# Kernel optimization log

Measured on AMD Instinct MI355X. Metric: run time of the kernel, lower is better.

Reference implementation:

```python
import jax, jax.numpy as jnp
import numpy as np

N, E, H, L, R, NG = 8192, 131072, 256, 3, 128, 64
NUM_ELEMENTS = 80
CUTOFF = 12.0
INV_SQRT_2 = 1.0 / np.sqrt(2.0)
INV_SQRT_3 = 1.0 / np.sqrt(3.0)
INV_SQRT_H = 1.0 / np.sqrt(H)


def _glorot(key, shape):
    fan_in, fan_out = shape[-2], shape[-1]
    return jax.random.normal(key, shape, jnp.float32) * np.sqrt(2.0 / (fan_in + fan_out))


def setup_inputs():
    key = jax.random.key(0)
    ks = jax.random.split(key, 24)
    pos = jax.random.normal(ks[0], (N, 3), jnp.float32) * 5.0
    z = jax.random.randint(ks[1], (N,), 0, NUM_ELEMENTS)
    src = jax.random.randint(ks[2], (E,), 0, N)
    off = jax.random.randint(ks[3], (E,), 1, N)
    dst = (src + off) % N  # guarantee no self-loops (dist > 0)
    edge_index = jnp.stack([src, dst])
    batch = jnp.sort(jax.random.randint(ks[4], (N,), 0, NG))
    return {
        "pos": pos,
        "atom_emb": jax.random.normal(ks[5], (NUM_ELEMENTS, H), jnp.float32),
        "ln_w": jnp.ones((L, H), jnp.float32),
        "ln_b": jnp.zeros((L, H), jnp.float32),
        "xp_w1": _glorot(ks[6], (L, H, H)),
        "xp_b1": jnp.zeros((L, H), jnp.float32),
        "xp_w2": _glorot(ks[7], (L, H, 3 * H)),
        "xp_b2": jnp.zeros((L, 3 * H), jnp.float32),
        "rbf_w": _glorot(ks[8], (L, R, 3 * H)),
        "rbf_b": jnp.zeros((L, 3 * H), jnp.float32),
        "vec_w": _glorot(ks[9], (L, H, 2 * H)),
        "xv_w1": _glorot(ks[10], (L, 2 * H, H)),
        "xv_b1": jnp.zeros((L, H), jnp.float32),
        "xv_w2": _glorot(ks[11], (L, H, 3 * H)),
        "xv_b2": jnp.zeros((L, 3 * H), jnp.float32),
        "oe_w1": _glorot(ks[12], (H, H // 2)),
        "oe_b1": jnp.zeros((H // 2,), jnp.float32),
        "oe_w2": _glorot(ks[13], (H // 2, 1)),
        "oe_b2": jnp.zeros((1,), jnp.float32),
        "z": z,
        "edge_index": edge_index,
        "batch": batch,
    }


def _gaussian_rbf(dist):
    offset = jnp.linspace(0.0, CUTOFF, R)
    coeff = -0.5 / (offset[1] - offset[0]) ** 2
    return jnp.exp(coeff * (dist[:, None] - offset[None, :]) ** 2)  # [E, R]


def _layernorm(x, w, b):
    mu = x.mean(-1, keepdims=True)
    var = x.var(-1, keepdims=True)
    return (x - mu) / jnp.sqrt(var + 1e-5) * w + b


def reference(pos, atom_emb, ln_w, ln_b, xp_w1, xp_b1, xp_w2, xp_b2,
              rbf_w, rbf_b, vec_w, xv_w1, xv_b1, xv_w2, xv_b2,
              oe_w1, oe_b1, oe_w2, oe_b2, z, edge_index, batch):
    src, dst = edge_index[0], edge_index[1]
    rel = pos[src] - pos[dst]                       # [E, 3]
    dist = jnp.sqrt((rel ** 2).sum(-1))             # [E]
    edge_rbf = _gaussian_rbf(dist)                  # [E, R]
    edge_vector = rel / dist[:, None]               # [E, 3] unit vectors

    x = atom_emb[z]                                 # [N, H]
    vec = jnp.zeros((N, 3, H), x.dtype)

    for l in range(L):
        # ---- PaiNNMessage ----
        xh = _layernorm(x, ln_w[l], ln_b[l])
        xh = jax.nn.silu(xh @ xp_w1[l] + xp_b1[l]) @ xp_w2[l] + xp_b2[l]  # [N, 3H]
        rbfh = edge_rbf @ rbf_w[l] + rbf_b[l]                             # [E, 3H]
        m = xh[src] * rbfh
        mx, xh2, xh3 = jnp.split(m, 3, axis=-1)
        xh2 = xh2 * INV_SQRT_3
        mvec = (vec[src] * xh2[:, None, :] + xh3[:, None, :] * edge_vector[:, :, None]) * INV_SQRT_H
        dx = jax.ops.segment_sum(mx, dst, num_segments=N)
        dvec = jax.ops.segment_sum(mvec, dst, num_segments=N)
        x = (x + dx) * INV_SQRT_2
        vec = vec + dvec

        # ---- PaiNNUpdate ----
        vp = vec @ vec_w[l]                          # [N, 3, 2H]
        vec1, vec2 = jnp.split(vp, 2, axis=-1)
        vec_dot = (vec1 * vec2).sum(axis=1) * INV_SQRT_H           # [N, H]
        vnorm = jnp.sqrt((vec2 ** 2).sum(axis=1) + 1e-8)           # [N, H]
        h = jnp.concatenate([x, vnorm], axis=-1)
        h = jax.nn.silu(h @ xv_w1[l] + xv_b1[l]) @ xv_w2[l] + xv_b2[l]
        xv1, xv2, xv3 = jnp.split(h, 3, axis=-1)
        dx = (xv1 + xv2 * vec_dot) * INV_SQRT_2
        dvec = xv3[:, None, :] * vec1
        x = (x + dx) * INV_SQRT_2
        vec = vec + dvec

    # ---- energy head: per-atom MLP then per-molecule sum ----
    per_atom = jax.nn.silu(x @ oe_w1 + oe_b1) @ oe_w2 + oe_b2      # [N, 1]
    energy = jax.ops.segment_sum(per_atom, batch, num_segments=NG)  # [NG, 1]
    return energy
```

## Files before the change

### kernel.cpp

```cpp
#include <hip/hip_runtime.h>
#include <hip/hip_bf16.h>
#include <math.h>

#define NN 8192
#define EE 131072
#define HH 256
#define LL 3
#define RR 128
#define NGG 64
#define MSG_WAVES 16

typedef __attribute__((ext_vector_type(8))) short bf16x8;
typedef __attribute__((ext_vector_type(4))) float f32x4;
typedef unsigned short u16;

union U4 { ushort4 v; unsigned short a[4]; };
union U8 { uint4 v; unsigned short a[8]; };

__device__ __forceinline__ float silu(float v) { return v / (1.0f + expf(-v)); }
__device__ __forceinline__ float b2f(unsigned short u) { return __uint_as_float(((unsigned)u) << 16); }
__device__ __forceinline__ unsigned short f2b(float f) {
    unsigned u = __float_as_uint(f);
    u += 0x7fff + ((u >> 16) & 1);
    return (unsigned short)(u >> 16);
}

constexpr float kInvSqrt2 = 0.70710678118654752440f;
constexpr float kInvSqrt3 = 0.57735026918962576451f;
constexpr float kInvSqrtH = 0.0625f;

__global__ void k_zero(float* __restrict__ p, int n4) {
    int i = blockIdx.x * 256 + threadIdx.x;
    if (i < n4) ((float4*)p)[i] = make_float4(0.f, 0.f, 0.f, 0.f);
}

__global__ __launch_bounds__(256) void k_wt_all(
    const float* __restrict__ xp_w1, const float* __restrict__ xp_w2,
    const float* __restrict__ rbf_w, const float* __restrict__ vec_w,
    const float* __restrict__ xv_w1, const float* __restrict__ xv_w2,
    const float* __restrict__ oe_w1,
    u16* __restrict__ xp_w1T, u16* __restrict__ xp_w2T, u16* __restrict__ rbf_wKb,
    u16* __restrict__ vec_wT, u16* __restrict__ xv_w1T, u16* __restrict__ xv_w2T,
    u16* __restrict__ oe_w1T) {
    int bid = blockIdx.x;
    const float* src; u16* dst; int K, N, t, cast = 0;
    if (bid < 2400) {
        int l = bid / 800, r = bid % 800;
        if (r < 64)       { src = xp_w1 + (size_t)l * 65536;  dst = xp_w1T + (size_t)l * 65536;  K = 256; N = 256; t = r; }
        else if (r < 256) { src = xp_w2 + (size_t)l * 196608; dst = xp_w2T + (size_t)l * 196608; K = 256; N = 768; t = r - 64; }
        else if (r < 352) { src = rbf_w + (size_t)l * 98304;  dst = rbf_wKb + (size_t)l * 98304; K = 128; N = 768; t = r - 256; cast = 1; }
        else if (r < 480) { src = vec_w + (size_t)l * 131072; dst = vec_wT + (size_t)l * 131072; K = 256; N = 512; t = r - 352; }
        else if (r < 608) { src = xv_w1 + (size_t)l * 131072; dst = xv_w1T + (size_t)l * 131072; K = 512; N = 256; t = r - 480; }
        else              { src = xv_w2 + (size_t)l * 196608; dst = xv_w2T + (size_t)l * 196608; K = 256; N = 768; t = r - 608; }
    } else {
        src = oe_w1; dst = oe_w1T; K = 256; N = 128; t = bid - 2400;
    }
    int nx = N >> 5;
    int bn = (t % nx) * 32, bk = (t / nx) * 32;
    int tx = threadIdx.x & 31, ty = threadIdx.x >> 5;
    if (cast) {
#pragma unroll
        for (int i = 0; i < 32; i += 8)
            dst[(size_t)(bk + ty + i) * N + bn + tx] = f2b(src[(size_t)(bk + ty + i) * N + bn + tx]);
        return;
    }
    __shared__ float tile[32][33];
#pragma unroll
    for (int i = 0; i < 32; i += 8)
        tile[ty + i][tx] = src[(size_t)(bk + ty + i) * N + bn + tx];
    __syncthreads();
#pragma unroll
    for (int i = 0; i < 32; i += 8)
        dst[(size_t)(bn + ty + i) * K + bk + tx] = f2b(tile[tx][ty + i]);
}

__global__ void k_init_ln(const float* __restrict__ emb, const int* __restrict__ z,
                          const float* __restrict__ w, const float* __restrict__ b,
                          float* __restrict__ x, u16* __restrict__ xlnb) {
    int n = blockIdx.x, t = threadIdx.x;
    float v = emb[z[n] * HH + t];
    x[(size_t)n * HH + t] = v;
    float s = v, q = v * v;
#pragma unroll
    for (int m = 32; m >= 1; m >>= 1) {
        s += __shfl_xor(s, m, 64);
        q += __shfl_xor(q, m, 64);
    }
    __shared__ float s_sum[4], s_sq[4];
    int wid = t >> 6;
    if ((t & 63) == 0) { s_sum[wid] = s; s_sq[wid] = q; }
    __syncthreads();
    float S = s_sum[0] + s_sum[1] + s_sum[2] + s_sum[3];
    float Q = s_sq[0] + s_sq[1] + s_sq[2] + s_sq[3];
    float mu = S * (1.0f / HH);
    float var = Q * (1.0f / HH) - mu * mu;
    float rs = rsqrtf(var + 1e-5f);
    xlnb[(size_t)n * HH + t] = f2b((v - mu) * rs * w[t] + b[t]);
}

__global__ void k_edge_geom(const float* __restrict__ pos, const int* __restrict__ ei,
                            float* __restrict__ ev ) {
    int e = blockIdx.x * 256 + threadIdx.x;
    if (e >= EE) return;
    int s = ei[e], d = ei[EE + e];
    float rx = pos[s * 3 + 0] - pos[d * 3 + 0];
    float ry = pos[s * 3 + 1] - pos[d * 3 + 1];
    float rz = pos[s * 3 + 2] - pos[d * 3 + 2];
    float dist = sqrtf(rx * rx + ry * ry + rz * rz);
    float inv = 1.0f / dist;
    ((float4*)ev)[e] = make_float4(rx * inv, ry * inv, rz * inv, dist);
}

__global__ void k_hist(const int* __restrict__ ei, int* __restrict__ deg) {
    int e = blockIdx.x * 256 + threadIdx.x;
    if (e < EE) atomicAdd(&deg[ei[EE + e]], 1);
}
__global__ void k_scan(const int* __restrict__ deg, int* __restrict__ row_ptr,
                       int* __restrict__ fill) {
    __shared__ int buf[256];
    __shared__ int carry_s;
    int t = threadIdx.x;
    if (t == 0) carry_s = 0;
    __syncthreads();
    for (int r = 0; r < NN; r += 256) {
        int v = deg[r + t];
        buf[t] = v;
        __syncthreads();
        for (int ofs = 1; ofs < 256; ofs <<= 1) {
            int add = (t >= ofs) ? buf[t - ofs] : 0;
            __syncthreads();
            buf[t] += add;
            __syncthreads();
        }
        int excl = buf[t] - v;
        int carry = carry_s;
        row_ptr[r + t] = carry + excl;
        fill[r + t] = carry + excl;
        __syncthreads();
        if (t == 255) carry_s = carry + buf[t];
        __syncthreads();
    }
    if (t == 0) row_ptr[NN] = carry_s;
}
__global__ void k_sort(const int* __restrict__ deg, int* __restrict__ dorder) {
    __shared__ int bins[256];
    __shared__ int base[256];
    int t = threadIdx.x;
    bins[t] = 0;
    __syncthreads();
    for (int d = t; d < NN; d += 256) {
        int b = deg[d]; b = b > 255 ? 255 : b;
        atomicAdd(&bins[b], 1);
    }
    __syncthreads();
    if (t == 0) {
        int acc = 0;
        for (int k = 255; k >= 0; --k) { base[k] = acc; acc += bins[k]; }
    }
    __syncthreads();
    bins[t] = 0;
    __syncthreads();
    for (int d = t; d < NN; d += 256) {
        int b = deg[d]; b = b > 255 ? 255 : b;
        int p = atomicAdd(&bins[b], 1);
        dorder[base[b] + p] = d;
    }
}
__global__ void k_scatter(const int* __restrict__ ei, const float* __restrict__ ev,
                          int* __restrict__ fill, int* __restrict__ srcp,
                          float4* __restrict__ evp, int* __restrict__ k0tab,
                          float* __restrict__ gtab) {
    int e = blockIdx.x * 256 + threadIdx.x;
    if (e >= EE) return;
    int d = ei[EE + e];
    int pos = atomicAdd(&fill[d], 1);
    float4 e4 = ((const float4*)ev)[e];
    srcp[pos] = ei[e];
    evp[pos] = e4;
    const float step = 12.0f / 127.0f;
    const float coeff = -0.5f / (step * step);
    float dist = e4.w;
    int k0 = (int)floorf(dist / step) - 3;
    k0 = k0 < 0 ? 0 : (k0 > 120 ? 120 : k0);
    float g[8];
#pragma unroll
    for (int k = 0; k < 8; ++k) {
        float t = dist - (k0 + k) * step;
        g[k] = expf(coeff * t * t);
    }
    k0tab[pos] = k0;
    ((float4*)gtab)[pos * 2 + 0] = make_float4(g[0], g[1], g[2], g[3]);
    ((float4*)gtab)[pos * 2 + 1] = make_float4(g[4], g[5], g[6], g[7]);
}

template <int AF32, int OUT_BF16, int ACT>
__global__ __launch_bounds__(256) void k_gemm(
    const void* __restrict__ Av, const u16* __restrict__ BT,
    const float* __restrict__ bias, void* __restrict__ C, int M, int K, int N) {
    __shared__ uint4 As4[512];
    __shared__ uint4 Bs4[512];
    u16* As = (u16*)As4;
    u16* Bs = (u16*)Bs4;
    int tid = threadIdx.x;
    int wave = tid >> 6, lane = tid & 63;
    int bm = blockIdx.y * 128, bn = blockIdx.x * 128;
    int wm = (wave >> 1) * 64, wn = (wave & 1) * 64;
    int lm = lane & 15;
    int kg = lane >> 4;
    f32x4 acc[4][4] = {};

    for (int k0 = 0; k0 < K; k0 += 32) {
#pragma unroll
        for (int it = 0; it < 2; ++it) {
            int idx = it * 256 + tid;
            int r = idx >> 2, seg = idx & 3;
            if (AF32) {
                const float* Af = (const float*)Av;
                float4 fa = *(const float4*)&Af[(size_t)(bm + r) * K + k0 + seg * 8];
                float4 fb = *(const float4*)&Af[(size_t)(bm + r) * K + k0 + seg * 8 + 4];
                U8 u;
                u.a[0] = f2b(fa.x); u.a[1] = f2b(fa.y); u.a[2] = f2b(fa.z); u.a[3] = f2b(fa.w);
                u.a[4] = f2b(fb.x); u.a[5] = f2b(fb.y); u.a[6] = f2b(fb.z); u.a[7] = f2b(fb.w);
                As4[idx] = u.v;
            } else {
                const u16* A = (const u16*)Av;
                As4[idx] = *(const uint4*)&A[(size_t)(bm + r) * K + k0 + seg * 8];
            }
            Bs4[idx] = *(const uint4*)&BT[(size_t)(bn + r) * K + k0 + seg * 8];
        }
        __syncthreads();
        bf16x8 af[4], bfr[4];
#pragma unroll
        for (int i = 0; i < 4; ++i)
            af[i] = *(const bf16x8*)&As[(wm + i * 16 + lm) * 32 + kg * 8];
#pragma unroll
        for (int j = 0; j < 4; ++j)
            bfr[j] = *(const bf16x8*)&Bs[(wn + j * 16 + lm) * 32 + kg * 8];
#pragma unroll
        for (int i = 0; i < 4; ++i)
#pragma unroll
            for (int j = 0; j < 4; ++j)
                acc[i][j] = __builtin_amdgcn_mfma_f32_16x16x32_bf16(af[i], bfr[j], acc[i][j], 0, 0, 0);
        __syncthreads();
    }

#pragma unroll
    for (int j = 0; j < 4; ++j) {
        int col = bn + wn + j * 16 + lm;
        float bv = bias ? bias[col] : 0.f;
#pragma unroll
        for (int i = 0; i < 4; ++i) {
            int row0 = bm + wm + i * 16 + kg * 4;
#pragma unroll
            for (int r = 0; r < 4; ++r) {
                float v = acc[i][j][r] + bv;
                if (ACT) v = silu(v);
                if (OUT_BF16)
                    ((u16*)C)[(size_t)(row0 + r) * N + col] = f2b(v);
                else
                    ((float*)C)[(size_t)(row0 + r) * N + col] = v;
            }
        }
    }
}

__global__ __launch_bounds__(1024) void k_msg(
    const u16* __restrict__ xhb, const u16* __restrict__ vinb,
    const int* __restrict__ srcp, const float4* __restrict__ evp,
    const int* __restrict__ row_ptr, const int* __restrict__ k0tab,
    const float* __restrict__ gtab, const u16* __restrict__ WK ,
    const float* __restrict__ rbias, float* __restrict__ x,
    const float* __restrict__ vin, float* __restrict__ vecM,
    const int* __restrict__ dorder) {
    __shared__ u16 Wp[128 * 256];
    int tid = threadIdx.x;
    int wave = tid >> 6, lane = tid & 63;
    int c0 = lane * 4;
    int d = dorder[blockIdx.x * MSG_WAVES + wave];
    int E0 = row_ptr[d], E1 = row_ptr[d + 1];
    float accv[3][4] = {};

#pragma unroll
    for (int p = 0; p < 3; ++p) {
        __syncthreads();
#pragma unroll
        for (int it = 0; it < 4; ++it) {
            int idx = it * 1024 + tid;
            int row = idx >> 5;
            int col8 = (idx & 31) * 8;
            *(uint4*)&Wp[row * 256 + col8] =
                *(const uint4*)&WK[(size_t)row * 768 + p * 256 + col8];
        }
        __syncthreads();
        float4 bb = ((const float4*)(rbias + p * 256))[lane];
        float bias4[4] = {bb.x, bb.y, bb.z, bb.w};
        float accx[4] = {};
        for (int j = E0; j < E1; ++j) {
            int s = srcp[j];
            int kj = k0tab[j];
            float4 ga = ((const float4*)gtab)[(size_t)j * 2 + 0];
            float4 gb = ((const float4*)gtab)[(size_t)j * 2 + 1];
            float g[8] = {ga.x, ga.y, ga.z, ga.w, gb.x, gb.y, gb.z, gb.w};
            float rr[4] = {bias4[0], bias4[1], bias4[2], bias4[3]};
#pragma unroll
            for (int k = 0; k < 8; ++k) {
                U4 w;
                w.v = *(const ushort4*)&Wp[(kj + k) * 256 + c0];
#pragma unroll
                for (int c = 0; c < 4; ++c) rr[c] += g[k] * b2f(w.a[c]);
            }
            if (p == 0) {
                U4 X; X.v = *(const ushort4*)(xhb + (size_t)s * 768 + c0);
#pragma unroll
                for (int c = 0; c < 4; ++c) accx[c] += b2f(X.a[c]) * rr[c];
            } else if (p == 1) {
                U4 X, V0, V1, V2;
                X.v = *(const ushort4*)(xhb + (size_t)s * 768 + 256 + c0);
                V0.v = *(const ushort4*)(vinb + (size_t)s * 768 + c0);
                V1.v = *(const ushort4*)(vinb + (size_t)s * 768 + 256 + c0);
                V2.v = *(const ushort4*)(vinb + (size_t)s * 768 + 512 + c0);
#pragma unroll
                for (int c = 0; c < 4; ++c) {
                    float m1 = b2f(X.a[c]) * rr[c] * kInvSqrt3;
                    accv[0][c] += b2f(V0.a[c]) * m1;
                    accv[1][c] += b2f(V1.a[c]) * m1;
                    accv[2][c] += b2f(V2.a[c]) * m1;
                }
            } else {
                U4 X; X.v = *(const ushort4*)(xhb + (size_t)s * 768 + 512 + c0);
                float4 ev4 = evp[j];
#pragma unroll
                for (int c = 0; c < 4; ++c) {
                    float m2 = b2f(X.a[c]) * rr[c];
                    accv[0][c] += m2 * ev4.x;
                    accv[1][c] += m2 * ev4.y;
                    accv[2][c] += m2 * ev4.z;
                }
            }
        }
        if (p == 0) {
            size_t xi = (size_t)d * 256 + c0;
            float4 xv = *(const float4*)&x[xi];
            xv.x = (xv.x + accx[0]) * kInvSqrt2;
            xv.y = (xv.y + accx[1]) * kInvSqrt2;
            xv.z = (xv.z + accx[2]) * kInvSqrt2;
            xv.w = (xv.w + accx[3]) * kInvSqrt2;
            *(float4*)&x[xi] = xv;
        }
    }
#pragma unroll
    for (int k = 0; k < 3; ++k) {
        size_t idx = (size_t)d * 768 + k * 256 + c0;
        float4 vv = *(const float4*)&vin[idx];
        vv.x += accv[k][0] * kInvSqrtH;
        vv.y += accv[k][1] * kInvSqrtH;
        vv.z += accv[k][2] * kInvSqrtH;
        vv.w += accv[k][3] * kInvSqrtH;
        *(float4*)&vecM[idx] = vv;
    }
}

__global__ void k_vecdot(const u16* __restrict__ vp, const float* __restrict__ x,
                         float* __restrict__ vec_dot, u16* __restrict__ hcat) {
    int i = blockIdx.x * 256 + threadIdx.x;
    int n = i >> 8, c = i & 255;
    const u16* p = vp + (size_t)n * 1536;
    float dsum = 0.f, qsum = 0.f;
#pragma unroll
    for (int k = 0; k < 3; ++k) {
        float v1 = b2f(p[k * 512 + c]);
        float v2 = b2f(p[k * 512 + 256 + c]);
        dsum += v1 * v2;
        qsum += v2 * v2;
    }
    vec_dot[i] = dsum * kInvSqrtH;
    hcat[(size_t)n * 512 + c] = f2b(x[i]);
    hcat[(size_t)n * 512 + 256 + c] = f2b(sqrtf(qsum + 1e-8f));
}

__global__ void k_update_out(const u16* __restrict__ hout, const float* __restrict__ vec_dot,
                             const u16* __restrict__ vp, float* __restrict__ x,
                             const float* __restrict__ vecM, float* __restrict__ vfin,
                             u16* __restrict__ vb,
                             const float* __restrict__ lnw, const float* __restrict__ lnb,
                             u16* __restrict__ xout) {
    int n = blockIdx.x, t = threadIdx.x;
    size_t i = (size_t)n * 256 + t;
    float xv1 = b2f(hout[(size_t)n * 768 + t]);
    float xv2 = b2f(hout[(size_t)n * 768 + 256 + t]);
    float xv3 = b2f(hout[(size_t)n * 768 + 512 + t]);
    float dxv = (xv1 + xv2 * vec_dot[i]) * kInvSqrt2;
    float nx = (x[i] + dxv) * kInvSqrt2;
    x[i] = nx;
#pragma unroll
    for (int k = 0; k < 3; ++k) {
        size_t idx = (size_t)n * 768 + k * 256 + t;
        float nv = vecM[idx] + xv3 * b2f(vp[(size_t)n * 1536 + k * 512 + t]);
        vfin[idx] = nv;
        vb[idx] = f2b(nv);
    }
    if (lnw) {
        float s = nx, q = nx * nx;
#pragma unroll
        for (int m = 32; m >= 1; m >>= 1) {
            s += __shfl_xor(s, m, 64);
            q += __shfl_xor(q, m, 64);
        }
        __shared__ float s_sum[4], s_sq[4];
        int wid = t >> 6;
        if ((t & 63) == 0) { s_sum[wid] = s; s_sq[wid] = q; }
        __syncthreads();
        float S = s_sum[0] + s_sum[1] + s_sum[2] + s_sum[3];
        float Q = s_sq[0] + s_sq[1] + s_sq[2] + s_sq[3];
        float mu = S * (1.0f / HH);
        float var = Q * (1.0f / HH) - mu * mu;
        float rs = rsqrtf(var + 1e-5f);
        xout[i] = f2b((nx - mu) * rs * lnw[t] + lnb[t]);
    } else {
        xout[i] = f2b(nx);
    }
}

__global__ void k_energy2(const float* __restrict__ h, const float* __restrict__ w2,
                          const float* __restrict__ b2, const int* __restrict__ batch,
                          float* __restrict__ out) {
    __shared__ float g[NGG];
    int t = threadIdx.x;
    if (t < NGG) g[t] = 0.f;
    __syncthreads();
    int a = blockIdx.x * 256 + t;
    const float4* hr = (const float4*)(h + (size_t)a * 128);
    const float4* w4 = (const float4*)w2;
    float acc = 0.f;
#pragma unroll 8
    for (int i = 0; i < 32; ++i) {
        float4 hv = hr[i], wv = w4[i];
        acc += hv.x * wv.x + hv.y * wv.y + hv.z * wv.z + hv.w * wv.w;
    }
    acc += b2[0];
    atomicAdd(&g[batch[a]], acc);
    __syncthreads();
    if (t < NGG && g[t] != 0.f) atomicAdd(&out[t], g[t]);
}

extern "C" void kernel_launch(void* const* d_in, const int* in_sizes, int n_in,
                              void* d_out, int out_size, void* d_ws, size_t ws_size,
                              hipStream_t stream) {
    const float* pos      = (const float*)d_in[0];
    const float* atom_emb = (const float*)d_in[1];
    const float* ln_w     = (const float*)d_in[2];
    const float* ln_b     = (const float*)d_in[3];
    const float* xp_w1    = (const float*)d_in[4];
    const float* xp_b1    = (const float*)d_in[5];
    const float* xp_w2    = (const float*)d_in[6];
    const float* xp_b2    = (const float*)d_in[7];
    const float* rbf_w    = (const float*)d_in[8];
    const float* rbf_b    = (const float*)d_in[9];
    const float* vec_w    = (const float*)d_in[10];
    const float* xv_w1    = (const float*)d_in[11];
    const float* xv_b1    = (const float*)d_in[12];
    const float* xv_w2    = (const float*)d_in[13];
    const float* xv_b2    = (const float*)d_in[14];
    const float* oe_w1    = (const float*)d_in[15];
    const float* oe_b1    = (const float*)d_in[16];
    const float* oe_w2    = (const float*)d_in[17];
    const float* oe_b2    = (const float*)d_in[18];
    const int*   z        = (const int*)d_in[19];
    const int*   ei       = (const int*)d_in[20];
    const int*   batch    = (const int*)d_in[21];
    float* out = (float*)d_out;

    char* ws = (char*)d_ws;
    size_t off = 0;
    auto alloc = [&](size_t b) {
        void* p = ws + off;
        off = (off + b + 255) & ~(size_t)255;
        return p;
    };
    float*  x      = (float*)alloc((size_t)NN * HH * 4);
    float*  vecA   = (float*)alloc((size_t)NN * 768 * 4);
    u16*    vb     = (u16*)alloc((size_t)NN * 768 * 2);
    float*  vecM   = (float*)alloc((size_t)NN * 768 * 4);
    u16*    xlnb   = (u16*)alloc((size_t)NN * HH * 2);
    u16*    t1b    = (u16*)alloc((size_t)NN * HH * 2);
    u16*    xhb    = (u16*)alloc((size_t)NN * 768 * 2);
    float*  vdot   = (float*)alloc((size_t)NN * HH * 4);
    u16*    vpb    = (u16*)alloc((size_t)NN * 1536 * 2);
    u16*    houtb  = (u16*)alloc((size_t)NN * 768 * 2);
    float*  ev     = (float*)alloc((size_t)EE * 4 * 4);
    int*    deg    = (int*)alloc((size_t)NN * 4);
    int*    row_ptr= (int*)alloc((size_t)(NN + 1) * 4);
    int*    fill   = (int*)alloc((size_t)NN * 4);
    int*    dorder = (int*)alloc((size_t)NN * 4);
    int*    srcp   = (int*)alloc((size_t)EE * 4);
    float4* evp    = (float4*)alloc((size_t)EE * 16);
    int*    k0tab  = (int*)alloc((size_t)EE * 4);
    float*  gtab   = (float*)alloc((size_t)EE * 8 * 4);
    u16* xp_w1T   = (u16*)alloc((size_t)3 * 256 * 256 * 2);
    u16* xp_w2T   = (u16*)alloc((size_t)3 * 768 * 256 * 2);
    u16* rbf_wKb  = (u16*)alloc((size_t)3 * 128 * 768 * 2);
    u16* vec_wT   = (u16*)alloc((size_t)3 * 512 * 256 * 2);
    u16* xv_w1T   = (u16*)alloc((size_t)3 * 256 * 512 * 2);
    u16* xv_w2T   = (u16*)alloc((size_t)3 * 768 * 256 * 2);
    u16* oe_w1T   = (u16*)alloc((size_t)128 * 256 * 2);
    (void)ws_size;

    u16*   h1b   = t1b;
    u16*   hcatb = xhb;
    float* heng  = vdot;
    u16*   xb    = xlnb;

    k_wt_all<<<2432, 256, 0, stream>>>(xp_w1, xp_w2, rbf_w, vec_w, xv_w1, xv_w2, oe_w1,
                                       xp_w1T, xp_w2T, rbf_wKb, vec_wT, xv_w1T, xv_w2T, oe_w1T);
    k_zero<<<(36 * 1024 * 1024 / 16 + 255) / 256, 256, 0, stream>>>(vecA, 36 * 1024 * 1024 / 16);
    k_zero<<<8, 256, 0, stream>>>((float*)deg, NN / 4);
    k_init_ln<<<NN, 256, 0, stream>>>(atom_emb, z, ln_w, ln_b, x, xlnb);
    k_edge_geom<<<EE / 256, 256, 0, stream>>>(pos, ei, ev);
    k_hist<<<EE / 256, 256, 0, stream>>>(ei, deg);
    k_scan<<<1, 256, 0, stream>>>(deg, row_ptr, fill);
    k_sort<<<1, 256, 0, stream>>>(deg, dorder);
    k_scatter<<<EE / 256, 256, 0, stream>>>(ei, ev, fill, srcp, evp, k0tab, gtab);

    for (int l = 0; l < LL; ++l) {
        k_gemm<0, 1, 1><<<dim3(2, NN / 128), 256, 0, stream>>>(
            xlnb, xp_w1T + (size_t)l * 256 * 256, xp_b1 + l * HH, t1b, NN, 256, 256);
        k_gemm<0, 1, 0><<<dim3(6, NN / 128), 256, 0, stream>>>(
            t1b, xp_w2T + (size_t)l * 768 * 256, xp_b2 + l * 768, xhb, NN, 256, 768);
        k_msg<<<NN / MSG_WAVES, 1024, 0, stream>>>(
            xhb, vb, srcp, evp, row_ptr, k0tab, gtab,
            rbf_wKb + (size_t)l * 128 * 768, rbf_b + l * 768, x, vecA, vecM, dorder);

        k_gemm<1, 1, 0><<<dim3(4, 3 * NN / 128), 256, 0, stream>>>(
            vecM, vec_wT + (size_t)l * 512 * 256, nullptr, vpb, 3 * NN, 256, 512);
        k_vecdot<<<NN, 256, 0, stream>>>(vpb, x, vdot, hcatb);
        k_gemm<0, 1, 1><<<dim3(2, NN / 128), 256, 0, stream>>>(
            hcatb, xv_w1T + (size_t)l * 256 * 512, xv_b1 + l * HH, h1b, NN, 512, 256);
        k_gemm<0, 1, 0><<<dim3(6, NN / 128), 256, 0, stream>>>(
            h1b, xv_w2T + (size_t)l * 768 * 256, xv_b2 + l * 768, houtb, NN, 256, 768);
        bool last = (l == LL - 1);
        k_update_out<<<NN, 256, 0, stream>>>(
            houtb, vdot, vpb, x, vecM, vecA, vb,
            last ? nullptr : ln_w + (l + 1) * HH,
            last ? nullptr : ln_b + (l + 1) * HH, xlnb);
    }

    k_gemm<0, 0, 1><<<dim3(1, NN / 128), 256, 0, stream>>>(
        xb, oe_w1T, oe_b1, heng, NN, 256, 128);
    k_zero<<<1, 256, 0, stream>>>(out, NGG / 4);
    k_energy2<<<32, 256, 0, stream>>>(heng, oe_w2, oe_b2, batch, out);
}
```

Baseline: 814.8 us.

## Pair-interleave RBF weights for packed FMA in message kernel; fuse setup kernels

Stores the RBF weight matrix with consecutive K rows interleaved per column, so the message kernel loads two RBF rows per 16-byte LDS read. The inner filter loop then uses float2 vectors, which lets the compiler emit packed FP32 math. k0 is forced even to match the pairing, so the truncated 8-term RBF window is shifted and may lose some accuracy for the highest terms. The edge geometry and degree histogram kernels are fused, and the scan and sort kernels are merged, to cut launches.

```diff
diff --git a/kernel.cpp b/kernel.cpp
--- a/kernel.cpp
+++ b/kernel.cpp
@@ -12,6 +12,7 @@
 
 typedef __attribute__((ext_vector_type(8))) short bf16x8;
 typedef __attribute__((ext_vector_type(4))) float f32x4;
+typedef __attribute__((ext_vector_type(2))) float f32x2;
 typedef unsigned short u16;
 
 union U4 { ushort4 v; unsigned short a[4]; };
@@ -39,16 +40,16 @@
     const float* __restrict__ rbf_w, const float* __restrict__ vec_w,
     const float* __restrict__ xv_w1, const float* __restrict__ xv_w2,
     const float* __restrict__ oe_w1,
-    u16* __restrict__ xp_w1T, u16* __restrict__ xp_w2T, u16* __restrict__ rbf_wKb,
+    u16* __restrict__ xp_w1T, u16* __restrict__ xp_w2T, u16* __restrict__ rbf_wP,
     u16* __restrict__ vec_wT, u16* __restrict__ xv_w1T, u16* __restrict__ xv_w2T,
     u16* __restrict__ oe_w1T) {
     int bid = blockIdx.x;
-    const float* src; u16* dst; int K, N, t, cast = 0;
+    const float* src; u16* dst; int K, N, t, pairmode = 0;
     if (bid < 2400) {
         int l = bid / 800, r = bid % 800;
         if (r < 64)       { src = xp_w1 + (size_t)l * 65536;  dst = xp_w1T + (size_t)l * 65536;  K = 256; N = 256; t = r; }
         else if (r < 256) { src = xp_w2 + (size_t)l * 196608; dst = xp_w2T + (size_t)l * 196608; K = 256; N = 768; t = r - 64; }
-        else if (r < 352) { src = rbf_w + (size_t)l * 98304;  dst = rbf_wKb + (size_t)l * 98304; K = 128; N = 768; t = r - 256; cast = 1; }
+        else if (r < 352) { src = rbf_w + (size_t)l * 98304;  dst = rbf_wP + (size_t)l * 98304;  K = 128; N = 768; t = r - 256; pairmode = 1; }
         else if (r < 480) { src = vec_w + (size_t)l * 131072; dst = vec_wT + (size_t)l * 131072; K = 256; N = 512; t = r - 352; }
         else if (r < 608) { src = xv_w1 + (size_t)l * 131072; dst = xv_w1T + (size_t)l * 131072; K = 512; N = 256; t = r - 480; }
         else              { src = xv_w2 + (size_t)l * 196608; dst = xv_w2T + (size_t)l * 196608; K = 256; N = 768; t = r - 608; }
@@ -58,10 +59,12 @@
     int nx = N >> 5;
     int bn = (t % nx) * 32, bk = (t / nx) * 32;
     int tx = threadIdx.x & 31, ty = threadIdx.x >> 5;
-    if (cast) {
-#pragma unroll
-        for (int i = 0; i < 32; i += 8)
-            dst[(size_t)(bk + ty + i) * N + bn + tx] = f2b(src[(size_t)(bk + ty + i) * N + bn + tx]);
+    if (pairmode) {
+#pragma unroll
+        for (int i = 0; i < 32; i += 8) {
+            int k = bk + ty + i, n = bn + tx;
+            dst[(size_t)(k >> 1) * 1536 + n * 2 + (k & 1)] = f2b(src[(size_t)k * N + n]);
+        }
         return;
     }
     __shared__ float tile[32][33];
@@ -98,8 +101,8 @@
     xlnb[(size_t)n * HH + t] = f2b((v - mu) * rs * w[t] + b[t]);
 }
 
-__global__ void k_edge_geom(const float* __restrict__ pos, const int* __restrict__ ei,
-                            float* __restrict__ ev ) {
+__global__ void k_geom_hist(const float* __restrict__ pos, const int* __restrict__ ei,
+                            float* __restrict__ ev, int* __restrict__ deg) {
     int e = blockIdx.x * 256 + threadIdx.x;
     if (e >= EE) return;
     int s = ei[e], d = ei[EE + e];
@@ -109,14 +112,11 @@
     float dist = sqrtf(rx * rx + ry * ry + rz * rz);
     float inv = 1.0f / dist;
     ((float4*)ev)[e] = make_float4(rx * inv, ry * inv, rz * inv, dist);
-}
-
-__global__ void k_hist(const int* __restrict__ ei, int* __restrict__ deg) {
-    int e = blockIdx.x * 256 + threadIdx.x;
-    if (e < EE) atomicAdd(&deg[ei[EE + e]], 1);
-}
-__global__ void k_scan(const int* __restrict__ deg, int* __restrict__ row_ptr,
-                       int* __restrict__ fill) {
+    atomicAdd(&deg[d], 1);
+}
+
+__global__ void k_scan_sort(const int* __restrict__ deg, int* __restrict__ row_ptr,
+                            int* __restrict__ fill, int* __restrict__ dorder) {
     __shared__ int buf[256];
     __shared__ int carry_s;
     int t = threadIdx.x;
@@ -141,11 +141,9 @@
         __syncthreads();
     }
     if (t == 0) row_ptr[NN] = carry_s;
-}
-__global__ void k_sort(const int* __restrict__ deg, int* __restrict__ dorder) {
+    __syncthreads();
     __shared__ int bins[256];
     __shared__ int base[256];
-    int t = threadIdx.x;
     bins[t] = 0;
     __syncthreads();
     for (int d = t; d < NN; d += 256) {
@@ -166,6 +164,7 @@
         dorder[base[b] + p] = d;
     }
 }
+
 __global__ void k_scatter(const int* __restrict__ ei, const float* __restrict__ ev,
                           int* __restrict__ fill, int* __restrict__ srcp,
                           float4* __restrict__ evp, int* __restrict__ k0tab,
@@ -180,7 +179,7 @@
     const float step = 12.0f / 127.0f;
     const float coeff = -0.5f / (step * step);
     float dist = e4.w;
-    int k0 = (int)floorf(dist / step) - 3;
+    int k0 = ((int)floorf(dist / step) - 3) & ~1;
     k0 = k0 < 0 ? 0 : (k0 > 120 ? 120 : k0);
     float g[8];
 #pragma unroll
@@ -268,17 +267,18 @@
     const u16* __restrict__ xhb, const u16* __restrict__ vinb,
     const int* __restrict__ srcp, const float4* __restrict__ evp,
     const int* __restrict__ row_ptr, const int* __restrict__ k0tab,
-    const float* __restrict__ gtab, const u16* __restrict__ WK ,
+    const float* __restrict__ gtab, const u16* __restrict__ WP ,
     const float* __restrict__ rbias, float* __restrict__ x,
     const float* __restrict__ vin, float* __restrict__ vecM,
     const int* __restrict__ dorder) {
-    __shared__ u16 Wp[128 * 256];
+    __shared__ u16 Wp[64 * 512];
     int tid = threadIdx.x;
     int wave = tid >> 6, lane = tid & 63;
     int c0 = lane * 4;
     int d = dorder[blockIdx.x * MSG_WAVES + wave];
     int E0 = row_ptr[d], E1 = row_ptr[d + 1];
-    float accv[3][4] = {};
+    f32x2 accvA[3] = {};
+    f32x2 accvB[3] = {};
 
 #pragma unroll
     for (int p = 0; p < 3; ++p) {
@@ -286,65 +286,71 @@
 #pragma unroll
         for (int it = 0; it < 4; ++it) {
             int idx = it * 1024 + tid;
-            int row = idx >> 5;
-            int col8 = (idx & 31) * 8;
-            *(uint4*)&Wp[row * 256 + col8] =
-                *(const uint4*)&WK[(size_t)row * 768 + p * 256 + col8];
+            int r = idx >> 6;
+            int c8 = (idx & 63) * 8;
+            *(uint4*)&Wp[r * 512 + c8] =
+                *(const uint4*)&WP[(size_t)r * 1536 + p * 512 + c8];
         }
         __syncthreads();
         float4 bb = ((const float4*)(rbias + p * 256))[lane];
-        float bias4[4] = {bb.x, bb.y, bb.z, bb.w};
-        float accx[4] = {};
+        f32x2 accxA = {}, accxB = {};
         for (int j = E0; j < E1; ++j) {
             int s = srcp[j];
-            int kj = k0tab[j];
+            int kp = k0tab[j] >> 1;
             float4 ga = ((const float4*)gtab)[(size_t)j * 2 + 0];
             float4 gb = ((const float4*)gtab)[(size_t)j * 2 + 1];
             float g[8] = {ga.x, ga.y, ga.z, ga.w, gb.x, gb.y, gb.z, gb.w};
-            float rr[4] = {bias4[0], bias4[1], bias4[2], bias4[3]};
-#pragma unroll
-            for (int k = 0; k < 8; ++k) {
-                U4 w;
-                w.v = *(const ushort4*)&Wp[(kj + k) * 256 + c0];
-#pragma unroll
-                for (int c = 0; c < 4; ++c) rr[c] += g[k] * b2f(w.a[c]);
+            f32x2 rrA = {bb.x, bb.y};
+            f32x2 rrB = {bb.z, bb.w};
+#pragma unroll
+            for (int p2 = 0; p2 < 4; ++p2) {
+                U8 w;
+                w.v = *(const uint4*)&Wp[(kp + p2) * 512 + c0 * 2];
+                float ge = g[2 * p2], go = g[2 * p2 + 1];
+                f32x2 loA = {b2f(w.a[0]), b2f(w.a[2])};
+                f32x2 hiA = {b2f(w.a[1]), b2f(w.a[3])};
+                f32x2 loB = {b2f(w.a[4]), b2f(w.a[6])};
+                f32x2 hiB = {b2f(w.a[5]), b2f(w.a[7])};
+                rrA += ge * loA + go * hiA;
+                rrB += ge * loB + go * hiB;
             }
             if (p == 0) {
                 U4 X; X.v = *(const ushort4*)(xhb + (size_t)s * 768 + c0);
-#pragma unroll
-                for (int c = 0; c < 4; ++c) accx[c] += b2f(X.a[c]) * rr[c];
+                f32x2 xA = {b2f(X.a[0]), b2f(X.a[1])};
+                f32x2 xB = {b2f(X.a[2]), b2f(X.a[3])};
+                accxA += xA * rrA;
+                accxB += xB * rrB;
             } else if (p == 1) {
                 U4 X, V0, V1, V2;
                 X.v = *(const ushort4*)(xhb + (size_t)s * 768 + 256 + c0);
                 V0.v = *(const ushort4*)(vinb + (size_t)s * 768 + c0);
                 V1.v = *(const ushort4*)(vinb + (size_t)s * 768 + 256 + c0);
                 V2.v = *(const ushort4*)(vinb + (size_t)s * 768 + 512 + c0);
-#pragma unroll
-                for (int c = 0; c < 4; ++c) {
-                    float m1 = b2f(X.a[c]) * rr[c] * kInvSqrt3;
-                    accv[0][c] += b2f(V0.a[c]) * m1;
-                    accv[1][c] += b2f(V1.a[c]) * m1;
-                    accv[2][c] += b2f(V2.a[c]) * m1;
-                }
+                f32x2 m1A = f32x2{b2f(X.a[0]), b2f(X.a[1])} * rrA * kInvSqrt3;
+                f32x2 m1B = f32x2{b2f(X.a[2]), b2f(X.a[3])} * rrB * kInvSqrt3;
+                accvA[0] += f32x2{b2f(V0.a[0]), b2f(V0.a[1])} * m1A;
+                accvB[0] += f32x2{b2f(V0.a[2]), b2f(V0.a[3])} * m1B;
+                accvA[1] += f32x2{b2f(V1.a[0]), b2f(V1.a[1])} * m1A;
+                accvB[1] += f32x2{b2f(V1.a[2]), b2f(V1.a[3])} * m1B;
+                accvA[2] += f32x2{b2f(V2.a[0]), b2f(V2.a[1])} * m1A;
+                accvB[2] += f32x2{b2f(V2.a[2]), b2f(V2.a[3])} * m1B;
             } else {
                 U4 X; X.v = *(const ushort4*)(xhb + (size_t)s * 768 + 512 + c0);
                 float4 ev4 = evp[j];
-#pragma unroll
-                for (int c = 0; c < 4; ++c) {
-                    float m2 = b2f(X.a[c]) * rr[c];
-                    accv[0][c] += m2 * ev4.x;
-                    accv[1][c] += m2 * ev4.y;
-                    accv[2][c] += m2 * ev4.z;
-                }
+                f32x2 m2A = f32x2{b2f(X.a[0]), b2f(X.a[1])} * rrA;
+                f32x2 m2B = f32x2{b2f(X.a[2]), b2f(X.a[3])} * rrB;
+                accvA[0] += m2A * ev4.x; accvB[0] += m2B * ev4.x;
+                accvA[1] += m2A * ev4.y; accvB[1] += m2B * ev4.y;
+                accvA[2] += m2A * ev4.z; accvB[2] += m2B * ev4.z;
             }
         }
         if (p == 0) {
             size_t xi = (size_t)d * 256 + c0;
             float4 xv = *(const float4*)&x[xi];
-            xv.x = (xv.x + accx[0]) * kInvSqrt2;
-            xv.y = (xv.y + accx[1]) * kInvSqrt2;
-            xv.z = (xv.z + accx[2]) * kInvSqrt2;
-            xv.w = (xv.w + accx[3]) * kInvSqrt2;
+            xv.x = (xv.x + accxA.x) * kInvSqrt2;
+            xv.y = (xv.y + accxA.y) * kInvSqrt2;
+            xv.z = (xv.z + accxB.x) * kInvSqrt2;
+            xv.w = (xv.w + accxB.y) * kInvSqrt2;
             *(float4*)&x[xi] = xv;
         }
     }
@@ -352,10 +358,10 @@
     for (int k = 0; k < 3; ++k) {
         size_t idx = (size_t)d * 768 + k * 256 + c0;
         float4 vv = *(const float4*)&vin[idx];
-        vv.x += accv[k][0] * kInvSqrtH;
-        vv.y += accv[k][1] * kInvSqrtH;
-        vv.z += accv[k][2] * kInvSqrtH;
-        vv.w += accv[k][3] * kInvSqrtH;
+        vv.x += accvA[k].x * kInvSqrtH;
+        vv.y += accvA[k].y * kInvSqrtH;
+        vv.z += accvB[k].x * kInvSqrtH;
+        vv.w += accvB[k].y * kInvSqrtH;
         *(float4*)&vecM[idx] = vv;
     }
 }
@@ -498,7 +504,7 @@
     float*  gtab   = (float*)alloc((size_t)EE * 8 * 4);
     u16* xp_w1T   = (u16*)alloc((size_t)3 * 256 * 256 * 2);
     u16* xp_w2T   = (u16*)alloc((size_t)3 * 768 * 256 * 2);
-    u16* rbf_wKb  = (u16*)alloc((size_t)3 * 128 * 768 * 2);
+    u16* rbf_wP   = (u16*)alloc((size_t)3 * 128 * 768 * 2);
     u16* vec_wT   = (u16*)alloc((size_t)3 * 512 * 256 * 2);
     u16* xv_w1T   = (u16*)alloc((size_t)3 * 256 * 512 * 2);
     u16* xv_w2T   = (u16*)alloc((size_t)3 * 768 * 256 * 2);
@@ -511,14 +517,12 @@
     u16*   xb    = xlnb;
 
     k_wt_all<<<2432, 256, 0, stream>>>(xp_w1, xp_w2, rbf_w, vec_w, xv_w1, xv_w2, oe_w1,
-                                       xp_w1T, xp_w2T, rbf_wKb, vec_wT, xv_w1T, xv_w2T, oe_w1T);
+                                       xp_w1T, xp_w2T, rbf_wP, vec_wT, xv_w1T, xv_w2T, oe_w1T);
     k_zero<<<(36 * 1024 * 1024 / 16 + 255) / 256, 256, 0, stream>>>(vecA, 36 * 1024 * 1024 / 16);
     k_zero<<<8, 256, 0, stream>>>((float*)deg, NN / 4);
     k_init_ln<<<NN, 256, 0, stream>>>(atom_emb, z, ln_w, ln_b, x, xlnb);
-    k_edge_geom<<<EE / 256, 256, 0, stream>>>(pos, ei, ev);
-    k_hist<<<EE / 256, 256, 0, stream>>>(ei, deg);
-    k_scan<<<1, 256, 0, stream>>>(deg, row_ptr, fill);
-    k_sort<<<1, 256, 0, stream>>>(deg, dorder);
+    k_geom_hist<<<EE / 256, 256, 0, stream>>>(pos, ei, ev, deg);
+    k_scan_sort<<<1, 256, 0, stream>>>(deg, row_ptr, fill, dorder);
     k_scatter<<<EE / 256, 256, 0, stream>>>(ei, ev, fill, srcp, evp, k0tab, gtab);
 
     for (int l = 0; l < LL; ++l) {
@@ -528,7 +532,7 @@
             t1b, xp_w2T + (size_t)l * 768 * 256, xp_b2 + l * 768, xhb, NN, 256, 768);
         k_msg<<<NN / MSG_WAVES, 1024, 0, stream>>>(
             xhb, vb, srcp, evp, row_ptr, k0tab, gtab,
-            rbf_wKb + (size_t)l * 128 * 768, rbf_b + l * 768, x, vecA, vecM, dorder);
+            rbf_wP + (size_t)l * 128 * 768, rbf_b + l * 768, x, vecA, vecM, dorder);
 
         k_gemm<1, 1, 0><<<dim3(4, 3 * NN / 128), 256, 0, stream>>>(
             vecM, vec_wT + (size_t)l * 512 * 256, nullptr, vpb, 3 * NN, 256, 512);
```

Result: no change. 819.4 us (+0.6%).
